# Optimization experiments

Hardware: AMD Instinct MI355X
Metric: run time of the kernel (lower is better)

The kernel has to match this reference:

```python
import jax, jax.numpy as jnp
import numpy as np

NUM_LAYERS, E, H = 4, 256, 8
HD = E // H
EPS = 1e-5


def _layer_norm(x, g, b):
    m = jnp.mean(x, axis=-1, keepdims=True)
    v = jnp.mean((x - m) ** 2, axis=-1, keepdims=True)
    return (x - m) / jnp.sqrt(v + EPS) * g + b


def _embed_rotary(x, pos):
    # x: [B, L, E], pos: [B, L, E, 2] (cos, sin)
    x2 = jnp.stack([-x[..., 1::2], x[..., ::2]], axis=-1).reshape(x.shape)
    return x * pos[..., 0] + x2 * pos[..., 1]


def setup_inputs() -> dict:
    key = jax.random.key(0)
    ks = jax.random.split(key, 16)
    Lq, B, Lkv = 512, 4, 4096
    s = 0.02
    return {
        "query": jax.random.normal(ks[0], (Lq, B, E), jnp.float32),
        "value": jax.random.normal(ks[1], (Lkv, B, E), jnp.float32),
        "query_pos": jax.random.normal(ks[2], (B, Lq, E, 2), jnp.float32),
        "value_pos": jax.random.normal(ks[3], (B, Lkv, E, 2), jnp.float32),
        "Wqkv": jax.random.normal(ks[4], (NUM_LAYERS, 3 * E, E), jnp.float32) * s,
        "bqkv": jnp.zeros((NUM_LAYERS, 3 * E), jnp.float32),
        "Wo": jax.random.normal(ks[5], (NUM_LAYERS, E, E), jnp.float32) * s,
        "bo": jnp.zeros((NUM_LAYERS, E), jnp.float32),
        "ln1_g": jnp.ones((NUM_LAYERS, E), jnp.float32),
        "ln1_b": jnp.zeros((NUM_LAYERS, E), jnp.float32),
        "W1": jax.random.normal(ks[6], (NUM_LAYERS, E, E), jnp.float32) * s,
        "b1": jnp.zeros((NUM_LAYERS, E), jnp.float32),
        "W2": jax.random.normal(ks[7], (NUM_LAYERS, E, E), jnp.float32) * s,
        "b2": jnp.zeros((NUM_LAYERS, E), jnp.float32),
        "ln2_g": jnp.ones((NUM_LAYERS, E), jnp.float32),
        "ln2_b": jnp.zeros((NUM_LAYERS, E), jnp.float32),
    }


def reference(query, value, query_pos, value_pos, Wqkv, bqkv, Wo, bo,
              ln1_g, ln1_b, W1, b1, W2, b2, ln2_g, ln2_b):
    Lq, B, _ = query.shape
    Lkv = value.shape[0]
    scale = HD ** -0.5

    def step(q_in, p):
        Wqkv_l, bqkv_l, Wo_l, bo_l, g1, be1, W1_l, b1_l, W2_l, b2_l, g2, be2 = p
        Wq, Wk, Wv = jnp.split(Wqkv_l, 3, axis=0)
        bq, bk, bv = jnp.split(bqkv_l, 3, axis=0)
        q = (q_in @ Wq.T + bq) * scale              # [Lq, B, E] (scaled as torch MHA)
        k = value @ Wk.T + bk                        # [Lkv, B, E]
        v = value @ Wv.T + bv
        qb = _embed_rotary(q.swapaxes(0, 1), query_pos)   # [B, Lq, E]
        kb = _embed_rotary(k.swapaxes(0, 1), value_pos)   # [B, Lkv, E]
        vb = v.swapaxes(0, 1)
        qh = qb.reshape(B, Lq, H, HD).transpose(0, 2, 1, 3)    # [B, H, Lq, HD]
        kh = kb.reshape(B, Lkv, H, HD).transpose(0, 2, 1, 3)
        vh = vb.reshape(B, Lkv, H, HD).transpose(0, 2, 1, 3)
        attn = jax.nn.softmax(jnp.einsum('bhqd,bhkd->bhqk', qh, kh), axis=-1)
        o = jnp.einsum('bhqk,bhkd->bhqd', attn, vh)            # [B, H, Lq, HD]
        o = o.transpose(0, 2, 1, 3).reshape(B, Lq, E).swapaxes(0, 1)  # [Lq, B, E]
        x = _layer_norm(q_in + o @ Wo_l.T + bo_l, g1, be1)
        ff = jax.nn.relu(x @ W1_l.T + b1_l) @ W2_l.T + b2_l
        y = _layer_norm(x + ff, g2, be2)
        return y, y

    params = (Wqkv, bqkv, Wo, bo, ln1_g, ln1_b, W1, b1, W2, b2, ln2_g, ln2_b)
    _, ys = jax.lax.scan(step, query, params)
    return ys  # [num_layers, Lq, B, E] — stacked per-layer outputs
```

## Files before the change

kernel.cpp:

```cpp
#include <hip/hip_runtime.h>
#include <hip/hip_bf16.h>

typedef __attribute__((ext_vector_type(8))) short short8;
typedef __attribute__((ext_vector_type(4))) float float4v;

#define LQ 512
#define NB 4
#define LKV 4096
#define E 256
#define NH 8
#define HD 32
#define NLAYER 4
#define QSCALE 0.17677669529663687f
#define SPLITS 8
#define KSPAN (LKV / SPLITS)
#define QT 128
#define CK 128

#define LDS_FENCE() asm volatile("s_waitcnt lgkmcnt(0)" ::: "memory")

__device__ __forceinline__ unsigned short f2bf(float f) {
    union { float f; unsigned int i; } x; x.f = f;
    unsigned int r = x.i + 0x7fffu + ((x.i >> 16) & 1u);
    return (unsigned short)(r >> 16);
}
__device__ __forceinline__ unsigned int pack2(float a, float b) {
    union { float f; unsigned int i; } xa, xb; xa.f = a; xb.f = b;
    unsigned int ra = xa.i + 0x7fffu + ((xa.i >> 16) & 1u);
    unsigned int rb = xb.i + 0x7fffu + ((xb.i >> 16) & 1u);
    return (ra >> 16) | (rb & 0xffff0000u);
}
__device__ __forceinline__ unsigned int pack2_rtz(float a, float b) {
    union { float f; unsigned int i; } xa, xb; xa.f = a; xb.f = b;
    return __builtin_amdgcn_perm(xb.i, xa.i, 0x07060302u);
}
__device__ __forceinline__ float bf2f(unsigned short u) {
    union { unsigned int i; float f; } x; x.i = ((unsigned int)u) << 16; return x.f;
}
__device__ __forceinline__ float4v mfma16(short8 a, short8 b, float4v c) {
    return __builtin_amdgcn_mfma_f32_16x16x32_bf16(a, b, c, 0, 0, 0);
}
__device__ __forceinline__ void pack_store8(const float* __restrict__ src,
                                            unsigned short* __restrict__ dst) {
    float4 a = *(const float4*)src;
    float4 b = *(const float4*)(src + 4);
    uint4 v;
    v.x = pack2(a.x, a.y); v.y = pack2(a.z, a.w);
    v.z = pack2(b.x, b.y); v.w = pack2(b.z, b.w);
    *(uint4*)dst = v;
}

__global__ void pack_all(const float* __restrict__ value, const float* __restrict__ Wqkv,
                         const float* __restrict__ Wo, const float* __restrict__ W1,
                         const float* __restrict__ W2, const float* __restrict__ qpos,
                         const float* __restrict__ vpos, const float* __restrict__ query,
                         unsigned short* __restrict__ val_t, unsigned short* __restrict__ wqkv_bf,
                         unsigned short* __restrict__ wo_bf, unsigned short* __restrict__ w1_bf,
                         unsigned short* __restrict__ w2_bf, unsigned short* __restrict__ qpos_bf,
                         unsigned short* __restrict__ vpos_bf, float* __restrict__ cur,
                         unsigned short* __restrict__ cur_bf) {
    int bid = blockIdx.x;
    if (bid < 2048) {
        long idx = ((long)bid * 256 + threadIdx.x) * 8;
        int ro = (int)(idx >> 8), e = (int)(idx & 255);
        int ri = ((ro & 4095) << 2) | (ro >> 12);
        pack_store8(value + (long)ri * 256 + e, val_t + idx);
        return;
    }
    bid -= 2048;
    if (bid < 384) { long i = ((long)bid * 256 + threadIdx.x) * 8; pack_store8(Wqkv + i, wqkv_bf + i); return; }
    bid -= 384;
    if (bid < 128) { long i = ((long)bid * 256 + threadIdx.x) * 8; pack_store8(Wo + i, wo_bf + i); return; }
    bid -= 128;
    if (bid < 128) { long i = ((long)bid * 256 + threadIdx.x) * 8; pack_store8(W1 + i, w1_bf + i); return; }
    bid -= 128;
    if (bid < 128) { long i = ((long)bid * 256 + threadIdx.x) * 8; pack_store8(W2 + i, w2_bf + i); return; }
    bid -= 128;
    if (bid < 512) { long i = ((long)bid * 256 + threadIdx.x) * 8; pack_store8(qpos + i, qpos_bf + i); return; }
    bid -= 512;
    if (bid < 4096) { long i = ((long)bid * 256 + threadIdx.x) * 8; pack_store8(vpos + i, vpos_bf + i); return; }
    bid -= 4096;
    {
        long i = ((long)bid * 256 + threadIdx.x) * 8;
        float4 a = *(const float4*)&query[i];
        float4 b = *(const float4*)&query[i + 4];
        *(float4*)&cur[i] = a;
        *(float4*)&cur[i + 4] = b;
        uint4 v;
        v.x = pack2(a.x, a.y); v.y = pack2(a.z, a.w);
        v.z = pack2(b.x, b.y); v.w = pack2(b.z, b.w);
        *(uint4*)&cur_bf[i] = v;
    }
}

__global__ __launch_bounds__(256) void gemm_k(
        const unsigned short* __restrict__ A, const unsigned short* __restrict__ W,
        const float* __restrict__ bias, unsigned short* __restrict__ out_bf) {
    __shared__ unsigned short sA[32 * 264];
    __shared__ unsigned short sB[64 * 264];
    const int t = threadIdx.x;
    const int lane = t & 63, wave = t >> 6, quad = lane >> 4, lid = lane & 15;
    const int row0 = blockIdx.x * 32, col0 = blockIdx.y * 64;
    {
        int r = t >> 3, ks = (t & 7) * 32;
        const unsigned short* ap = A + (long)(row0 + r) * E + ks;
#pragma unroll
        for (int i = 0; i < 4; i++)
            *(uint4*)&sA[r * 264 + ks + i * 8] = *(const uint4*)(ap + i * 8);
    }
    {
        int r = t >> 2, ks = (t & 3) * 64;
        const unsigned short* wp = W + (long)(col0 + r) * E + ks;
#pragma unroll
        for (int i = 0; i < 8; i++)
            *(uint4*)&sB[r * 264 + ks + i * 8] = *(const uint4*)(wp + i * 8);
    }
    __syncthreads();
    float4v acc[2];
    acc[0] = (float4v){0.f, 0.f, 0.f, 0.f};
    acc[1] = (float4v){0.f, 0.f, 0.f, 0.f};
#pragma unroll
    for (int k0 = 0; k0 < E; k0 += 32) {
        short8 bf = *(const short8*)&sB[(wave * 16 + lid) * 264 + k0 + quad * 8];
        short8 af0 = *(const short8*)&sA[(lid) * 264 + k0 + quad * 8];
        short8 af1 = *(const short8*)&sA[(16 + lid) * 264 + k0 + quad * 8];
        acc[0] = mfma16(af0, bf, acc[0]);
        acc[1] = mfma16(af1, bf, acc[1]);
    }
#pragma unroll
    for (int mt = 0; mt < 2; mt++)
#pragma unroll
        for (int r = 0; r < 4; r++) {
            int grow = row0 + mt * 16 + quad * 4 + r;
            int gcol = col0 + wave * 16 + lid;
            float v = fmaxf(acc[mt][r] + bias[gcol], 0.f);
            out_bf[(long)grow * E + gcol] = f2bf(v);
        }
}

template <int COMBINE, int OUT2>
__global__ __launch_bounds__(256, 1) void gemm_ln(
        const unsigned short* __restrict__ A,
        const float* __restrict__ Opart, const float* __restrict__ lp,
        const unsigned short* __restrict__ W, const float* __restrict__ bias,
        const float* __restrict__ res, const float* __restrict__ g,
        const float* __restrict__ bvec, float* __restrict__ outf,
        unsigned short* __restrict__ out_bf, float* __restrict__ outf2) {
    __shared__ unsigned short sA[16 * 264];
    __shared__ float lnS[4][16];
    __shared__ float lnQ[4][16];
    const int t = threadIdx.x;
    const int lane = t & 63, wave = t >> 6, quad = lane >> 4, lid = lane & 15;
    const int row0 = blockIdx.x * 16;
    {
        const int r = t >> 4, cseg = t & 15;
        if (COMBINE) {
            const int grow = row0 + r;
            const int seq = grow >> 2, b = grow & 3;
            const int h = cseg >> 1, dd = (cseg & 1) * 16;
            const int bh = b * 8 + h;
            float L = 0.f;
            float av[16];
#pragma unroll
            for (int j = 0; j < 16; j++) av[j] = 0.f;
#pragma unroll
            for (int s = 0; s < SPLITS; s++) {
                long rbase = (long)(s * 32 + bh) * 512 + seq;
                L += lp[rbase];
#pragma unroll
                for (int jj = 0; jj < 4; jj++) {
                    float4 p = *(const float4*)&Opart[rbase * 32 + dd + jj * 4];
                    av[jj * 4 + 0] += p.x; av[jj * 4 + 1] += p.y;
                    av[jj * 4 + 2] += p.z; av[jj * 4 + 3] += p.w;
                }
            }
            float inv = 1.f / L;
            uint4 u0, u1;
            u0.x = pack2(av[0] * inv, av[1] * inv);   u0.y = pack2(av[2] * inv, av[3] * inv);
            u0.z = pack2(av[4] * inv, av[5] * inv);   u0.w = pack2(av[6] * inv, av[7] * inv);
            u1.x = pack2(av[8] * inv, av[9] * inv);   u1.y = pack2(av[10] * inv, av[11] * inv);
            u1.z = pack2(av[12] * inv, av[13] * inv); u1.w = pack2(av[14] * inv, av[15] * inv);
            *(uint4*)&sA[r * 264 + cseg * 16] = u0;
            *(uint4*)&sA[r * 264 + cseg * 16 + 8] = u1;
        } else {
            const unsigned short* ap = A + (long)(row0 + r) * E + cseg * 16;
            *(uint4*)&sA[r * 264 + cseg * 16] = *(const uint4*)ap;
            *(uint4*)&sA[r * 264 + cseg * 16 + 8] = *(const uint4*)(ap + 8);
        }
    }
    __syncthreads();
    float4v acc[4];
#pragma unroll
    for (int nf = 0; nf < 4; nf++) acc[nf] = (float4v){0.f, 0.f, 0.f, 0.f};
#pragma unroll
    for (int k0 = 0; k0 < E; k0 += 32) {
        short8 af = *(const short8*)&sA[lid * 264 + k0 + quad * 8];
#pragma unroll
        for (int nf = 0; nf < 4; nf++) {
            short8 bf = *(const short8*)(W + (long)(wave * 64 + nf * 16 + lid) * E + k0 + quad * 8);
            acc[nf] = mfma16(af, bf, acc[nf]);
        }
    }
    float v[4][4];
    float sr[4], qr_[4];
#pragma unroll
    for (int r = 0; r < 4; r++) { sr[r] = 0.f; qr_[r] = 0.f; }
#pragma unroll
    for (int nf = 0; nf < 4; nf++) {
        int col = wave * 64 + nf * 16 + lid;
        float bcol = bias[col];
#pragma unroll
        for (int r = 0; r < 4; r++) {
            int grow = row0 + quad * 4 + r;
            float val = acc[nf][r] + bcol + res[(long)grow * E + col];
            v[nf][r] = val;
            sr[r] += val;
            qr_[r] += val * val;
        }
    }
#pragma unroll
    for (int r = 0; r < 4; r++) {
#pragma unroll
        for (int d = 1; d < 16; d <<= 1) {
            sr[r] += __shfl_xor(sr[r], d);
            qr_[r] += __shfl_xor(qr_[r], d);
        }
    }
    if (lid == 0) {
#pragma unroll
        for (int r = 0; r < 4; r++) {
            lnS[wave][quad * 4 + r] = sr[r];
            lnQ[wave][quad * 4 + r] = qr_[r];
        }
    }
    __syncthreads();
    float mean[4], rstd[4];
#pragma unroll
    for (int r = 0; r < 4; r++) {
        int row = quad * 4 + r;
        float S = lnS[0][row] + lnS[1][row] + lnS[2][row] + lnS[3][row];
        float Q = lnQ[0][row] + lnQ[1][row] + lnQ[2][row] + lnQ[3][row];
        float mu = S * (1.f / 256.f);
        float var = Q * (1.f / 256.f) - mu * mu;
        mean[r] = mu;
        rstd[r] = rsqrtf(var + 1e-5f);
    }
#pragma unroll
    for (int nf = 0; nf < 4; nf++) {
        int col = wave * 64 + nf * 16 + lid;
        float gc = g[col], bc = bvec[col];
#pragma unroll
        for (int r = 0; r < 4; r++) {
            int grow = row0 + quad * 4 + r;
            float xo = (v[nf][r] - mean[r]) * rstd[r] * gc + bc;
            outf[(long)grow * E + col] = xo;
            out_bf[(long)grow * E + col] = f2bf(xo);
            if (OUT2) outf2[(long)grow * E + col] = xo;
        }
    }
}

__global__ __launch_bounds__(256) void qkv_q(
        const unsigned short* __restrict__ A, const unsigned short* __restrict__ W,
        const float* __restrict__ bias, const unsigned short* __restrict__ pos,
        unsigned short* __restrict__ qout) {
    __shared__ unsigned short sA[32 * 40];
    __shared__ unsigned short sB[64 * 40];
    const int t = threadIdx.x;
    const int lane = t & 63, wave = t >> 6, quad = lane >> 4, lid = lane & 15;
    const int row0 = blockIdx.x * 32, col0 = blockIdx.y * 64;
    const int sr = t >> 2, sk = (t & 3) * 8;
    const unsigned short* ap = A + (long)(row0 + sr) * E + sk;
    const unsigned short* wp = W + (long)(col0 + sr) * E + sk;
    uint4 av, bv;
    if (t < 128) av = *(const uint4*)ap;
    bv = *(const uint4*)wp;
    float4v acc[2];
    acc[0] = (float4v){0.f, 0.f, 0.f, 0.f};
    acc[1] = (float4v){0.f, 0.f, 0.f, 0.f};
#pragma unroll
    for (int ki = 0; ki < 8; ki++) {
        __syncthreads();
        if (t < 128) *(uint4*)&sA[sr * 40 + sk] = av;
        *(uint4*)&sB[sr * 40 + sk] = bv;
        __syncthreads();
        if (ki < 7) {
            if (t < 128) av = *(const uint4*)(ap + (ki + 1) * 32);
            bv = *(const uint4*)(wp + (ki + 1) * 32);
        }
        short8 af0 = *(const short8*)&sA[lid * 40 + quad * 8];
        short8 af1 = *(const short8*)&sA[(16 + lid) * 40 + quad * 8];
        short8 bf = *(const short8*)&sB[(wave * 16 + lid) * 40 + quad * 8];
        acc[0] = mfma16(af0, bf, acc[0]);
        acc[1] = mfma16(af1, bf, acc[1]);
    }
#pragma unroll
    for (int mt = 0; mt < 2; mt++)
#pragma unroll
        for (int r = 0; r < 4; r++) {
            int grow = row0 + mt * 16 + quad * 4 + r;
            int gcol = col0 + wave * 16 + lid;
            float v = (acc[mt][r] + bias[gcol]) * QSCALE;
            int seq = grow >> 2, b = grow & 3;
            int c = gcol;
            unsigned int cs = *(const unsigned int*)&pos[(((long)b * LQ + seq) * E + c) * 2];
            float cv = bf2f((unsigned short)cs), sv = bf2f((unsigned short)(cs >> 16));
            float p = __shfl_xor(v, 1);
            float x2 = (c & 1) ? p : -p;
            float rv = v * cv + x2 * sv;
            qout[(((long)b * NH + (c >> 5)) * LQ + seq) * HD + (c & 31)] = f2bf(rv);
        }
}

__global__ __launch_bounds__(256) void qkv_kv(
        const unsigned short* __restrict__ A, const unsigned short* __restrict__ Wall,
        const float* __restrict__ ball, const unsigned short* __restrict__ pos,
        unsigned short* __restrict__ kall, unsigned short* __restrict__ vtall) {
    const int layer = blockIdx.z;
    const unsigned short* W = Wall + (long)layer * 768 * 256 + 256 * 256;
    const float* bias = ball + (long)layer * 768 + 256;
    unsigned short* kout = kall + (long)layer * 4194304;
    unsigned short* vtout = vtall + (long)layer * 4194304;
    __shared__ unsigned short sA[64 * 72];
    __shared__ unsigned short sB[64 * 72];
    __shared__ unsigned short sT[64 * 72];
    const int t = threadIdx.x;
    const int lane = t & 63, wave = t >> 6, quad = lane >> 4, lid = lane & 15;
    const int wr = wave >> 1, wc = wave & 1;
    const int row0 = blockIdx.x * 64, col0 = blockIdx.y * 64;
    const int b = row0 >> 12, seq0 = row0 & 4095;
    const int r = t >> 2, kk = (t & 3) * 16;
    const unsigned short* apg = A + (long)(row0 + r) * E + kk;
    const unsigned short* wpg = W + (long)(col0 + r) * E + kk;
    uint4 a0 = *(const uint4*)apg,        a1 = *(const uint4*)(apg + 8);
    uint4 b0 = *(const uint4*)wpg,        b1 = *(const uint4*)(wpg + 8);
    float4v acc[2][2];
    for (int i = 0; i < 2; i++) for (int j = 0; j < 2; j++) acc[i][j] = (float4v){0.f, 0.f, 0.f, 0.f};
#pragma unroll
    for (int ki = 0; ki < 4; ki++) {
        __syncthreads();
        *(uint4*)&sA[r * 72 + kk] = a0; *(uint4*)&sA[r * 72 + kk + 8] = a1;
        *(uint4*)&sB[r * 72 + kk] = b0; *(uint4*)&sB[r * 72 + kk + 8] = b1;
        __syncthreads();
        if (ki < 3) {
            a0 = *(const uint4*)(apg + (ki + 1) * 64); a1 = *(const uint4*)(apg + (ki + 1) * 64 + 8);
            b0 = *(const uint4*)(wpg + (ki + 1) * 64); b1 = *(const uint4*)(wpg + (ki + 1) * 64 + 8);
        }
#pragma unroll
        for (int kf = 0; kf < 2; kf++) {
            const int ko = kf * 32 + quad * 8;
            short8 af0 = *(const short8*)&sA[(wr * 32 + lid) * 72 + ko];
            short8 af1 = *(const short8*)&sA[(wr * 32 + 16 + lid) * 72 + ko];
            short8 bf0 = *(const short8*)&sB[(wc * 32 + lid) * 72 + ko];
            short8 bf1 = *(const short8*)&sB[(wc * 32 + 16 + lid) * 72 + ko];
            acc[0][0] = mfma16(af0, bf0, acc[0][0]);
            acc[0][1] = mfma16(af0, bf1, acc[0][1]);
            acc[1][0] = mfma16(af1, bf0, acc[1][0]);
            acc[1][1] = mfma16(af1, bf1, acc[1][1]);
        }
    }
    if (col0 < 256) {
#pragma unroll
        for (int mt = 0; mt < 2; mt++)
#pragma unroll
            for (int nt = 0; nt < 2; nt++)
#pragma unroll
                for (int rr = 0; rr < 4; rr++) {
                    int m = wr * 32 + mt * 16 + quad * 4 + rr;
                    int c = col0 + wc * 32 + nt * 16 + lid;
                    int seq = seq0 + m;
                    float v = acc[mt][nt][rr] + bias[c];
                    unsigned int cs = *(const unsigned int*)&pos[(((long)b * LKV + seq) * E + c) * 2];
                    float cv = bf2f((unsigned short)cs), sv = bf2f((unsigned short)(cs >> 16));
                    float p = __shfl_xor(v, 1);
                    float x2 = (c & 1) ? p : -p;
                    float rv = v * cv + x2 * sv;
                    kout[(((long)b * NH + (c >> 5)) * LKV + seq) * HD + (c & 31)] = f2bf(rv);
                }
    } else {
#pragma unroll
        for (int mt = 0; mt < 2; mt++)
#pragma unroll
            for (int nt = 0; nt < 2; nt++) {
                int cl = wc * 32 + nt * 16 + lid;
                int so = wr * 32 + mt * 16 + quad * 4;
                float bcol = bias[col0 + cl];
                uint2 pw;
                pw.x = pack2(acc[mt][nt][0] + bcol, acc[mt][nt][1] + bcol);
                pw.y = pack2(acc[mt][nt][2] + bcol, acc[mt][nt][3] + bcol);
                *(uint2*)&sT[cl * 72 + so] = pw;
            }
        __syncthreads();
        const int cl = t >> 2, sc = (t & 3) * 16;
        uint4 u0 = *(const uint4*)&sT[cl * 72 + sc];
        uint4 u1 = *(const uint4*)&sT[cl * 72 + sc + 8];
        int cg = (col0 - 256) + cl;
        unsigned short* dst = vtout + (((long)b * NH + (cg >> 5)) * HD + (cg & 31)) * (long)LKV + seq0 + sc;
        *(uint4*)dst = u0;
        *(uint4*)(dst + 8) = u1;
    }
}

__global__ __launch_bounds__(256) void attn_k(
        const unsigned short* __restrict__ qb, const unsigned short* __restrict__ kb,
        const unsigned short* __restrict__ vtb, float* __restrict__ Opart,
        float* __restrict__ lpart) {
    __shared__ unsigned short sK[CK * 40];
    __shared__ unsigned short sVT[32 * 136];
    __shared__ unsigned short sPT[4 * 64 * 36];
    const int t = threadIdx.x;
    const int lane = t & 63, wave = t >> 6, quad = lane >> 4, lid = lane & 15;
    const int qt0 = blockIdx.x * QT;
    const int bh = blockIdx.y;
    const int key0 = blockIdx.z * KSPAN;
    const unsigned short* kbase = kb + (long)bh * LKV * HD;
    const unsigned short* vbase = vtb + (long)bh * HD * LKV;
    short8 aq[2];
#pragma unroll
    for (int mf = 0; mf < 2; mf++)
        aq[mf] = *(const short8*)(qb + ((long)bh * LQ + qt0 + wave * 32 + mf * 16 + lid) * HD + quad * 8);
    float4v o[2][2];
#pragma unroll
    for (int i = 0; i < 2; i++) for (int j = 0; j < 2; j++) o[i][j] = (float4v){0.f, 0.f, 0.f, 0.f};
    float l[8] = {0.f, 0.f, 0.f, 0.f, 0.f, 0.f, 0.f, 0.f};
    const int krow = t >> 1, khalf = (t & 1) * 16;
    const int vrow = t >> 3, vkoff = (t & 7) * 16;
    unsigned short* myPT = &sPT[wave * 64 * 36];
    uint4 kv0 = *(const uint4*)(kbase + (long)(key0 + krow) * HD + khalf);
    uint4 kv1 = *(const uint4*)(kbase + (long)(key0 + krow) * HD + khalf + 8);
    uint4 vv0 = *(const uint4*)(vbase + (long)vrow * LKV + key0 + vkoff);
    uint4 vv1 = *(const uint4*)(vbase + (long)vrow * LKV + key0 + vkoff + 8);
    for (int ck = key0; ck < key0 + KSPAN; ck += CK) {
        __syncthreads();
        *(uint4*)&sK[krow * 40 + khalf] = kv0;
        *(uint4*)&sK[krow * 40 + khalf + 8] = kv1;
        *(uint4*)&sVT[vrow * 136 + vkoff] = vv0;
        *(uint4*)&sVT[vrow * 136 + vkoff + 8] = vv1;
        __syncthreads();
        if (ck + CK < key0 + KSPAN) {
            kv0 = *(const uint4*)(kbase + (long)(ck + CK + krow) * HD + khalf);
            kv1 = *(const uint4*)(kbase + (long)(ck + CK + krow) * HD + khalf + 8);
            vv0 = *(const uint4*)(vbase + (long)vrow * LKV + ck + CK + vkoff);
            vv1 = *(const uint4*)(vbase + (long)vrow * LKV + ck + CK + vkoff + 8);
        }
#pragma unroll
        for (int half = 0; half < 2; half++) {
#pragma unroll
            for (int nf = 0; nf < 4; nf++) {
                short8 bk = *(const short8*)&sK[(half * 64 + nf * 16 + lid) * 40 + quad * 8];
#pragma unroll
                for (int mf = 0; mf < 2; mf++) {
                    float4v z = (float4v){0.f, 0.f, 0.f, 0.f};
                    float4v s = mfma16(aq[mf], bk, z);
                    float e0 = __expf(s[0]), e1 = __expf(s[1]);
                    float e2 = __expf(s[2]), e3 = __expf(s[3]);
                    l[mf * 4 + 0] += e0; l[mf * 4 + 1] += e1;
                    l[mf * 4 + 2] += e2; l[mf * 4 + 3] += e3;
                    uint2 pk;
                    pk.x = pack2_rtz(e0, e1);
                    pk.y = pack2_rtz(e2, e3);
                    *(uint2*)&myPT[(nf * 16 + lid) * 36 + mf * 16 + quad * 4] = pk;
                }
            }
            LDS_FENCE();
#pragma unroll
            for (int kb2 = 0; kb2 < 2; kb2++) {
                short8 bv0 = *(const short8*)&sVT[lid * 136 + half * 64 + kb2 * 32 + quad * 8];
                short8 bv1 = *(const short8*)&sVT[(16 + lid) * 136 + half * 64 + kb2 * 32 + quad * 8];
#pragma unroll
                for (int mf = 0; mf < 2; mf++) {
                    short8 ap;
#pragma unroll
                    for (int j = 0; j < 8; j++)
                        ap[j] = (short)myPT[(kb2 * 32 + quad * 8 + j) * 36 + mf * 16 + lid];
                    o[mf][0] = mfma16(ap, bv0, o[mf][0]);
                    o[mf][1] = mfma16(ap, bv1, o[mf][1]);
                }
            }
            LDS_FENCE();
        }
    }
#pragma unroll
    for (int i = 0; i < 8; i++) {
#pragma unroll
        for (int d = 1; d < 16; d <<= 1) l[i] += __shfl_xor(l[i], d);
    }
#pragma unroll
    for (int mf = 0; mf < 2; mf++)
#pragma unroll
        for (int r = 0; r < 4; r++) {
            long orow = ((long)blockIdx.z * 32 + bh) * LQ + qt0 + wave * 32 + mf * 16 + quad * 4 + r;
            Opart[orow * HD + lid] = o[mf][0][r];
            Opart[orow * HD + 16 + lid] = o[mf][1][r];
            if (lid == 0) lpart[orow] = l[mf * 4 + r];
        }
}

extern "C" void kernel_launch(void* const* d_in, const int* in_sizes, int n_in,
                              void* d_out, int out_size, void* d_ws, size_t ws_size,
                              hipStream_t stream) {
    (void)in_sizes; (void)n_in; (void)out_size; (void)ws_size;
    const float* query = (const float*)d_in[0];
    const float* value = (const float*)d_in[1];
    const float* qpos  = (const float*)d_in[2];
    const float* vpos  = (const float*)d_in[3];
    const float* Wqkv  = (const float*)d_in[4];
    const float* bqkv  = (const float*)d_in[5];
    const float* Wo    = (const float*)d_in[6];
    const float* bo    = (const float*)d_in[7];
    const float* g1    = (const float*)d_in[8];
    const float* be1   = (const float*)d_in[9];
    const float* W1    = (const float*)d_in[10];
    const float* b1    = (const float*)d_in[11];
    const float* W2    = (const float*)d_in[12];
    const float* b2    = (const float*)d_in[13];
    const float* g2    = (const float*)d_in[14];
    const float* be2   = (const float*)d_in[15];
    float* outp = (float*)d_out;

    char* w = (char*)d_ws;
    float*          cur     = (float*)(w + 0);
    unsigned short* cur_bf  = (unsigned short*)(w + (2l  << 20));
    unsigned short* qbuf    = (unsigned short*)(w + (3l  << 20));
    float*          xb      = (float*)(w + (4l  << 20));
    unsigned short* xb_bf   = (unsigned short*)(w + (6l  << 20));
    unsigned short* h1b_bf  = (unsigned short*)(w + (7l  << 20));
    float*          lp      = (float*)(w + (8l  << 20));
    float*          Opart   = (float*)(w + (9l  << 20));
    unsigned short* val_t   = (unsigned short*)(w + (25l << 20));
    unsigned short* wqkv_bf = (unsigned short*)(w + (33l << 20));
    unsigned short* wo_bf   = (unsigned short*)(w + (35l << 20));
    unsigned short* w1_bf   = (unsigned short*)(w + (36l << 20));
    unsigned short* w2_bf   = (unsigned short*)(w + (37l << 20));
    unsigned short* qpos_bf = (unsigned short*)(w + (38l << 20));
    unsigned short* vpos_bf = (unsigned short*)(w + (40l << 20));
    unsigned short* kbuf    = (unsigned short*)(w + (56l << 20));
    unsigned short* vtb     = (unsigned short*)(w + (88l << 20));

    pack_all<<<7680, 256, 0, stream>>>(value, Wqkv, Wo, W1, W2, qpos, vpos, query,
                                       val_t, wqkv_bf, wo_bf, w1_bf, w2_bf, qpos_bf,
                                       vpos_bf, cur, cur_bf);

    qkv_kv<<<dim3(256, 8, NLAYER), 256, 0, stream>>>(val_t, wqkv_bf, bqkv, vpos_bf, kbuf, vtb);

    for (int layer = 0; layer < NLAYER; layer++) {
        const unsigned short* Wl = wqkv_bf + (long)layer * 768 * 256;
        const float* bl = bqkv + (long)layer * 768;
        qkv_q<<<dim3(64, 4), 256, 0, stream>>>(cur_bf, Wl, bl, qpos_bf, qbuf);
        attn_k<<<dim3(LQ / QT, 32, SPLITS), 256, 0, stream>>>(
            qbuf, kbuf + (long)layer * 4194304, vtb + (long)layer * 4194304, Opart, lp);
        gemm_ln<1, 0><<<128, 256, 0, stream>>>(
            nullptr, Opart, lp, wo_bf + layer * 65536, bo + layer * 256,
            cur, g1 + layer * 256, be1 + layer * 256, xb, xb_bf, nullptr);
        gemm_k<<<dim3(64, 4), 256, 0, stream>>>(xb_bf, w1_bf + layer * 65536, b1 + layer * 256, h1b_bf);
        gemm_ln<0, 1><<<128, 256, 0, stream>>>(
            h1b_bf, nullptr, nullptr, w2_bf + layer * 65536, b2 + layer * 256,
            xb, g2 + layer * 256, be2 + layer * 256, cur, cur_bf,
            outp + (long)layer * LQ * NB * E);
    }
}
```

Measured before the change: 379.4 us.

## Store attention partials in bf16, prefetch gemm_ln weights to registers, share qkv_kv LDS

Attention split partial outputs are now written as bf16 instead of fp32, halving the bytes moved between the attention kernel and the combine step in gemm_ln. gemm_ln loads its whole weight slice into registers before the A-tile staging so the global loads overlap the combine work, and preloads A fragments from LDS before the MFMA loop. qkv_kv reuses one LDS buffer for the transpose tile to cut shared memory use. The cost is lower precision in the partial sums and higher register pressure in gemm_ln.

After: 359.4 us. 1.06x faster.

```diff
diff --git a/kernel.cpp b/kernel.cpp
--- a/kernel.cpp
+++ b/kernel.cpp
@@ -141,7 +141,7 @@
 template <int COMBINE, int OUT2>
 __global__ __launch_bounds__(256, 1) void gemm_ln(
         const unsigned short* __restrict__ A,
-        const float* __restrict__ Opart, const float* __restrict__ lp,
+        const unsigned short* __restrict__ Opart, const float* __restrict__ lp,
         const unsigned short* __restrict__ W, const float* __restrict__ bias,
         const float* __restrict__ res, const float* __restrict__ g,
         const float* __restrict__ bvec, float* __restrict__ outf,
@@ -152,6 +152,12 @@
     const int t = threadIdx.x;
     const int lane = t & 63, wave = t >> 6, quad = lane >> 4, lid = lane & 15;
     const int row0 = blockIdx.x * 16;
+    short8 wreg[8][4];
+#pragma unroll
+    for (int k0 = 0; k0 < 8; k0++)
+#pragma unroll
+        for (int nf = 0; nf < 4; nf++)
+            wreg[k0][nf] = *(const short8*)(W + (long)(wave * 64 + nf * 16 + lid) * E + k0 * 32 + quad * 8);
     {
         const int r = t >> 4, cseg = t & 15;
         if (COMBINE) {
@@ -167,12 +173,17 @@
             for (int s = 0; s < SPLITS; s++) {
                 long rbase = (long)(s * 32 + bh) * 512 + seq;
                 L += lp[rbase];
-#pragma unroll
-                for (int jj = 0; jj < 4; jj++) {
-                    float4 p = *(const float4*)&Opart[rbase * 32 + dd + jj * 4];
-                    av[jj * 4 + 0] += p.x; av[jj * 4 + 1] += p.y;
-                    av[jj * 4 + 2] += p.z; av[jj * 4 + 3] += p.w;
-                }
+                const unsigned short* op = Opart + rbase * 32 + dd;
+                uint4 u0 = *(const uint4*)op;
+                uint4 u1 = *(const uint4*)(op + 8);
+                av[0]  += bf2f((unsigned short)u0.x); av[1]  += bf2f((unsigned short)(u0.x >> 16));
+                av[2]  += bf2f((unsigned short)u0.y); av[3]  += bf2f((unsigned short)(u0.y >> 16));
+                av[4]  += bf2f((unsigned short)u0.z); av[5]  += bf2f((unsigned short)(u0.z >> 16));
+                av[6]  += bf2f((unsigned short)u0.w); av[7]  += bf2f((unsigned short)(u0.w >> 16));
+                av[8]  += bf2f((unsigned short)u1.x); av[9]  += bf2f((unsigned short)(u1.x >> 16));
+                av[10] += bf2f((unsigned short)u1.y); av[11] += bf2f((unsigned short)(u1.y >> 16));
+                av[12] += bf2f((unsigned short)u1.z); av[13] += bf2f((unsigned short)(u1.z >> 16));
+                av[14] += bf2f((unsigned short)u1.w); av[15] += bf2f((unsigned short)(u1.w >> 16));
             }
             float inv = 1.f / L;
             uint4 u0, u1;
@@ -189,18 +200,18 @@
         }
     }
     __syncthreads();
+    short8 ar[8];
+#pragma unroll
+    for (int k0 = 0; k0 < 8; k0++)
+        ar[k0] = *(const short8*)&sA[lid * 264 + k0 * 32 + quad * 8];
     float4v acc[4];
 #pragma unroll
     for (int nf = 0; nf < 4; nf++) acc[nf] = (float4v){0.f, 0.f, 0.f, 0.f};
 #pragma unroll
-    for (int k0 = 0; k0 < E; k0 += 32) {
-        short8 af = *(const short8*)&sA[lid * 264 + k0 + quad * 8];
-#pragma unroll
-        for (int nf = 0; nf < 4; nf++) {
-            short8 bf = *(const short8*)(W + (long)(wave * 64 + nf * 16 + lid) * E + k0 + quad * 8);
-            acc[nf] = mfma16(af, bf, acc[nf]);
-        }
-    }
+    for (int k0 = 0; k0 < 8; k0++)
+#pragma unroll
+        for (int nf = 0; nf < 4; nf++)
+            acc[nf] = mfma16(ar[k0], wreg[k0][nf], acc[nf]);
     float v[4][4];
     float sr[4], qr_[4];
 #pragma unroll
@@ -241,9 +252,8 @@
         float S = lnS[0][row] + lnS[1][row] + lnS[2][row] + lnS[3][row];
         float Q = lnQ[0][row] + lnQ[1][row] + lnQ[2][row] + lnQ[3][row];
         float mu = S * (1.f / 256.f);
-        float var = Q * (1.f / 256.f) - mu * mu;
         mean[r] = mu;
-        rstd[r] = rsqrtf(var + 1e-5f);
+        rstd[r] = rsqrtf(Q * (1.f / 256.f) - mu * mu + 1e-5f);
     }
 #pragma unroll
     for (int nf = 0; nf < 4; nf++) {
@@ -321,9 +331,9 @@
     const float* bias = ball + (long)layer * 768 + 256;
     unsigned short* kout = kall + (long)layer * 4194304;
     unsigned short* vtout = vtall + (long)layer * 4194304;
-    __shared__ unsigned short sA[64 * 72];
-    __shared__ unsigned short sB[64 * 72];
-    __shared__ unsigned short sT[64 * 72];
+    __shared__ unsigned short smem[2 * 64 * 72];
+    unsigned short* sA = smem;
+    unsigned short* sB = smem + 64 * 72;
     const int t = threadIdx.x;
     const int lane = t & 63, wave = t >> 6, quad = lane >> 4, lid = lane & 15;
     const int wr = wave >> 1, wc = wave & 1;
@@ -378,6 +388,8 @@
                     kout[(((long)b * NH + (c >> 5)) * LKV + seq) * HD + (c & 31)] = f2bf(rv);
                 }
     } else {
+        __syncthreads();
+        unsigned short* sT = smem;
 #pragma unroll
         for (int mt = 0; mt < 2; mt++)
 #pragma unroll
@@ -403,7 +415,7 @@
 
 __global__ __launch_bounds__(256) void attn_k(
         const unsigned short* __restrict__ qb, const unsigned short* __restrict__ kb,
-        const unsigned short* __restrict__ vtb, float* __restrict__ Opart,
+        const unsigned short* __restrict__ vtb, unsigned short* __restrict__ Opart,
         float* __restrict__ lpart) {
     __shared__ unsigned short sK[CK * 40];
     __shared__ unsigned short sVT[32 * 136];
@@ -490,8 +502,9 @@
 #pragma unroll
         for (int r = 0; r < 4; r++) {
             long orow = ((long)blockIdx.z * 32 + bh) * LQ + qt0 + wave * 32 + mf * 16 + quad * 4 + r;
-            Opart[orow * HD + lid] = o[mf][0][r];
-            Opart[orow * HD + 16 + lid] = o[mf][1][r];
+            unsigned short* ob = Opart + orow * HD;
+            ob[lid] = f2bf(o[mf][0][r]);
+            ob[16 + lid] = f2bf(o[mf][1][r]);
             if (lid == 0) lpart[orow] = l[mf * 4 + r];
         }
 }
@@ -526,7 +539,7 @@
     unsigned short* xb_bf   = (unsigned short*)(w + (6l  << 20));
     unsigned short* h1b_bf  = (unsigned short*)(w + (7l  << 20));
     float*          lp      = (float*)(w + (8l  << 20));
-    float*          Opart   = (float*)(w + (9l  << 20));
+    unsigned short* Opart   = (unsigned short*)(w + (9l  << 20));
     unsigned short* val_t   = (unsigned short*)(w + (25l << 20));
     unsigned short* wqkv_bf = (unsigned short*)(w + (33l << 20));
     unsigned short* wo_bf   = (unsigned short*)(w + (35l << 20));
```
